# Performance work log

Hardware: AMD Instinct MI355X
Metric: run time of the kernel (lower is better)

## Reference

```python
import jax, jax.numpy as jnp
import numpy as np

HIDDEN = 2048
NUM_HEADS = 16
NUM_KV_HEADS = 4
HEAD_DIM = HIDDEN // NUM_HEADS  # 128
GROUP = NUM_HEADS // NUM_KV_HEADS  # 4
SCALE = HEAD_DIM ** -0.5


def setup_inputs() -> dict:
    key = jax.random.key(0)
    ks = jax.random.split(key, 9)
    B, S = 2, 2048
    kv_dim = HEAD_DIM * NUM_KV_HEADS
    std = HIDDEN ** -0.5
    return {
        "x": jax.random.normal(ks[0], (B, S, HIDDEN), dtype=jnp.float32),
        "Wq": jax.random.normal(ks[1], (HIDDEN, HIDDEN), dtype=jnp.float32) * std,
        "bq": jnp.zeros((HIDDEN,), dtype=jnp.float32),
        "Wk": jax.random.normal(ks[2], (HIDDEN, kv_dim), dtype=jnp.float32) * std,
        "bk": jnp.zeros((kv_dim,), dtype=jnp.float32),
        "Wv": jax.random.normal(ks[3], (HIDDEN, kv_dim), dtype=jnp.float32) * std,
        "bv": jnp.zeros((kv_dim,), dtype=jnp.float32),
        "Wo": jax.random.normal(ks[4], (HIDDEN, HIDDEN), dtype=jnp.float32) * std,
        "bo": jnp.zeros((HIDDEN,), dtype=jnp.float32),
    }


def reference(x, Wq, bq, Wk, bk, Wv, bv, Wo, bo):
    B, S, _ = x.shape
    # projections
    q = (x @ Wq + bq).reshape(B, S, NUM_KV_HEADS, GROUP, HEAD_DIM)  # grouped query heads
    k = (x @ Wk + bk).reshape(B, S, NUM_KV_HEADS, HEAD_DIM)
    v = (x @ Wv + bv).reshape(B, S, NUM_KV_HEADS, HEAD_DIM)
    # scores: [B, Hkv, G, Sq, Sk] -- same math as repeat_interleave of K/V over G,
    # but K/V are broadcast over the group axis instead of materialized.
    attn = jnp.einsum("bqhgd,bkhd->bhgqk", q, k) * SCALE
    attn = jax.nn.softmax(attn, axis=-1)
    out = jnp.einsum("bhgqk,bkhd->bqhgd", attn, v).reshape(B, S, HIDDEN)
    return out @ Wo + bo
```

## Files before the change

kernel.cpp:

```cpp
#include <hip/hip_runtime.h>


#define SEQ    2048
#define HIDDEN 2048

typedef __attribute__((ext_vector_type(8))) short v8s;
typedef __attribute__((ext_vector_type(4))) float v4f;

#define MFMA16(a,b,c) __builtin_amdgcn_mfma_f32_16x16x32_bf16((a),(b),(c),0,0,0)

__device__ __forceinline__ ushort f2b(float f){
  unsigned u = __float_as_uint(f);
  u += 0x7fffu + ((u >> 16) & 1u);
  return (ushort)(u >> 16);
}

__device__ __forceinline__ unsigned cvt_pk_bf16(float lo, float hi){
  unsigned r;
  asm("v_cvt_pk_bf16_f32 %0, %1, %2" : "=v"(r) : "v"(lo), "v"(hi));
  return r;
}

__device__ __forceinline__ void gload16(const void* g, void* l){
  __builtin_amdgcn_global_load_lds((const __attribute__((address_space(1))) void*)g,
                                   (__attribute__((address_space(3))) void*)l, 16, 0, 0);
}

#define WAIT_VM0   0x0F70
#define WAIT_VM2   0x0F72
#define WAIT_LGKM0 0xC07F

__global__ void k_conv(const float* __restrict__ in, ushort* __restrict__ out, int n){
  int i = (blockIdx.x*256 + threadIdx.x)*4;
  if (i >= n) return;
  float4 f = *(const float4*)(in + i);
  ushort4 u; u.x=f2b(f.x); u.y=f2b(f.y); u.z=f2b(f.z); u.w=f2b(f.w);
  *(ushort4*)(out + i) = u;
}

__global__ void k_tconv(const float* __restrict__ in, ushort* __restrict__ out,
                        int rows, int cols){
  __shared__ float t[32][33];
  int tx = threadIdx.x & 31, ty = threadIdx.x >> 5;
  int c0 = blockIdx.x*32, r0 = blockIdx.y*32;
#pragma unroll
  for (int i=0;i<4;i++) t[ty+i*8][tx] = in[(size_t)(r0+ty+i*8)*cols + c0+tx];
  __syncthreads();
#pragma unroll
  for (int i=0;i<4;i++) out[(size_t)(c0+ty+i*8)*rows + r0+tx] = f2b(t[tx][ty+i*8]);
}

__global__ void k_tv(const ushort* __restrict__ vb, ushort* __restrict__ vT){
  __shared__ ushort t[32][33];
  int tx = threadIdx.x & 31, ty = threadIdx.x >> 5;
  int s0 = blockIdx.x*32, d0 = blockIdx.y*32, bh = blockIdx.z;
  int b = bh >> 2, h = bh & 3;
  const ushort* src = vb + (size_t)b*SEQ*512 + h*128;
#pragma unroll
  for (int i=0;i<4;i++) t[ty+i*8][tx] = src[(size_t)(s0+ty+i*8)*512 + d0+tx];
  __syncthreads();
  ushort* dst = vT + (size_t)bh*128*SEQ;
#pragma unroll
  for (int i=0;i<4;i++) dst[(size_t)(d0+ty+i*8)*SEQ + s0+tx] = t[tx][ty+i*8];
}

#define GEMM256_MAIN(A_, Bt_)                                                          \
  __shared__ ushort sA[2][2][128*64], sB[2][2][128*64];                                \
  const int tid = threadIdx.x, lane = tid & 63, w = tid >> 6;                          \
  const int wm = w >> 2, wn = w & 3, lm = lane & 15, quad = lane >> 4;                 \
  const int wh = wn >> 1, wl = wn & 1, l3 = lane >> 3, l7m = lm & 7;                   \
  const int swz = ((lane & 7) ^ (l3 & 7)) * 8;                                         \
  const ushort* Ag = (A_); const ushort* Bg = (Bt_);                                   \
  v4f acc[8][4] = {};                                                                  \
  STG_A(0,0,0) STG_A(0,1,0) STG_B(0,0,0) STG_B(0,1,0) STG_A(1,0,1)                     \
  __builtin_amdgcn_s_waitcnt(WAIT_VM2);                                                \
  __builtin_amdgcn_s_barrier(); __builtin_amdgcn_sched_barrier(0);                     \
  for (int t = 0; t < 32; t++){                                                        \
    const int p = t & 1, pn = p ^ 1;                                                   \
    const int tn  = (t+1 < 32) ? t+1 : t;                                              \
    const int tnn = (t+2 < 32) ? t+2 : 31;                                             \
    v8s a0[4][2], a1[4][2], bb0[2][2], bb1[2][2];                                      \
                                                                              \
    _Pragma("unroll")                                                                  \
    for (int i=0;i<4;i++){ LDA(a0[i][0], i, 0) LDA(a0[i][1], i, 1) }                   \
    _Pragma("unroll")                                                                  \
    for (int j=0;j<2;j++){ LDB(bb0[j][0], j, 0) LDB(bb0[j][1], j, 1) }                 \
    STG_A(tn, 1, pn)                                                                   \
    __builtin_amdgcn_s_barrier(); __builtin_amdgcn_sched_barrier(0);                   \
    __builtin_amdgcn_s_waitcnt(WAIT_LGKM0); __builtin_amdgcn_sched_barrier(0);         \
    __builtin_amdgcn_s_setprio(1);                                                     \
    _Pragma("unroll")                                                                  \
    for (int ks=0;ks<2;ks++)                                                           \
      _Pragma("unroll")                                                                \
      for (int i=0;i<4;i++)                                                            \
        _Pragma("unroll")                                                              \
        for (int j=0;j<2;j++) acc[i][j] = MFMA16(a0[i][ks], bb0[j][ks], acc[i][j]);    \
    __builtin_amdgcn_s_setprio(0);                                                     \
    __builtin_amdgcn_s_barrier(); __builtin_amdgcn_sched_barrier(0);                   \
                                                                              \
    _Pragma("unroll")                                                                  \
    for (int j=0;j<2;j++){ LDB(bb1[j][0], j+2, 0) LDB(bb1[j][1], j+2, 1) }             \
    STG_B(tn, 0, pn)                                                                   \
    __builtin_amdgcn_s_barrier(); __builtin_amdgcn_sched_barrier(0);                   \
    __builtin_amdgcn_s_waitcnt(WAIT_LGKM0); __builtin_amdgcn_sched_barrier(0);         \
    __builtin_amdgcn_s_setprio(1);                                                     \
    _Pragma("unroll")                                                                  \
    for (int ks=0;ks<2;ks++)                                                           \
      _Pragma("unroll")                                                                \
      for (int i=0;i<4;i++)                                                            \
        _Pragma("unroll")                                                              \
        for (int j=0;j<2;j++) acc[i][j+2] = MFMA16(a0[i][ks], bb1[j][ks], acc[i][j+2]);\
    __builtin_amdgcn_s_setprio(0);                                                     \
    __builtin_amdgcn_s_barrier(); __builtin_amdgcn_sched_barrier(0);                   \
                                                                              \
    _Pragma("unroll")                                                                  \
    for (int i=0;i<4;i++){ LDA(a1[i][0], i+4, 0) LDA(a1[i][1], i+4, 1) }               \
    STG_B(tn, 1, pn)                                                                   \
    __builtin_amdgcn_s_barrier(); __builtin_amdgcn_sched_barrier(0);                   \
    __builtin_amdgcn_s_waitcnt(WAIT_LGKM0); __builtin_amdgcn_sched_barrier(0);         \
    __builtin_amdgcn_s_setprio(1);                                                     \
    _Pragma("unroll")                                                                  \
    for (int ks=0;ks<2;ks++)                                                           \
      _Pragma("unroll")                                                                \
      for (int i=0;i<4;i++)                                                            \
        _Pragma("unroll")                                                              \
        for (int j=0;j<2;j++) acc[i+4][j] = MFMA16(a1[i][ks], bb0[j][ks], acc[i+4][j]);\
    __builtin_amdgcn_s_setprio(0);                                                     \
    __builtin_amdgcn_s_barrier(); __builtin_amdgcn_sched_barrier(0);                   \
                  \
    STG_A(tnn, 0, p)                                                                   \
    __builtin_amdgcn_s_waitcnt(WAIT_VM2); __builtin_amdgcn_sched_barrier(0);           \
    __builtin_amdgcn_s_barrier(); __builtin_amdgcn_sched_barrier(0);                   \
    __builtin_amdgcn_s_setprio(1);                                                     \
    _Pragma("unroll")                                                                  \
    for (int ks=0;ks<2;ks++)                                                           \
      _Pragma("unroll")                                                                \
      for (int i=0;i<4;i++)                                                            \
        _Pragma("unroll")                                                              \
        for (int j=0;j<2;j++)                                                          \
          acc[i+4][j+2] = MFMA16(a1[i][ks], bb1[j][ks], acc[i+4][j+2]);                \
    __builtin_amdgcn_s_setprio(0);                                                     \
    __builtin_amdgcn_s_barrier(); __builtin_amdgcn_sched_barrier(0);                   \
  }

#define STG_A(t_, h_, buf_) { _Pragma("unroll") for (int i_=0;i_<2;i_++){              \
    int c_ = w*2 + i_;                                                                 \
    gload16(Ag + (size_t)(rowB + (h_)*128 + c_*8 + l3)*HIDDEN + (t_)*64 + swz,         \
            &sA[buf_][h_][c_*512 + lane*8]); } }
#define STG_B(t_, h_, buf_) { _Pragma("unroll") for (int i_=0;i_<2;i_++){              \
    int c_ = w*2 + i_;                                                                 \
    gload16(Bg + (size_t)(colB + (h_)*128 + c_*8 + l3)*HIDDEN + (t_)*64 + swz,         \
            &sB[buf_][h_][c_*512 + lane*8]); } }
#define LDA(dst_, i_, ks_) dst_ = *(const v8s*)(&sA[p][wm][((i_)*16+lm)*64 + ((((ks_)*4+quad))^l7m)*8]);
#define LDB(dst_, j_, ks_) dst_ = *(const v8s*)(&sB[p][wh][(wl*64 + (j_)*16+lm)*64 + ((((ks_)*4+quad))^l7m)*8]);

__global__ __launch_bounds__(512, 1) void k_gemm_qkv(
    const ushort* __restrict__ A, const ushort* __restrict__ Bt,
    const float* __restrict__ bq, const float* __restrict__ bk, const float* __restrict__ bv,
    ushort* __restrict__ qb, ushort* __restrict__ kb, ushort* __restrict__ vb){
  const int flat = blockIdx.x;
  const int nf = (flat & 7) * 24 + (flat >> 3);
  const int rowB = (nf & 15) * 256;
  const int colB = (nf >> 4) * 256;
  GEMM256_MAIN(A, Bt)
#pragma unroll
  for (int i=0;i<8;i++)
#pragma unroll
  for (int j=0;j<4;j++){
    int col = colB + wn*64 + j*16 + lm;
#pragma unroll
    for (int r=0;r<4;r++){
      int row = rowB + wm*128 + i*16 + quad*4 + r;
      float v = acc[i][j][r];
      if (col < 2048)      qb[(size_t)row*2048 + col]        = f2b(v + bq[col]);
      else if (col < 2560) kb[(size_t)row*512 + (col-2048)]  = f2b(v + bk[col-2048]);
      else                 vb[(size_t)row*512 + (col-2560)]  = f2b(v + bv[col-2560]);
    }
  }
}

__global__ __launch_bounds__(512, 1) void k_gemm_out(
    const ushort* __restrict__ A, const ushort* __restrict__ Bt,
    const float* __restrict__ bo, float* __restrict__ out){
  __shared__ ushort sA[2][128*64], sB[2][2][128*64];
  const int tid = threadIdx.x, lane = tid & 63, w = tid >> 6;
  const int wm = w >> 2, wn = w & 3, lm = lane & 15, quad = lane >> 4;
  const int wh = wn >> 1, wl = wn & 1, l3 = lane >> 3, l7m = lm & 7;
  const int swz = ((lane & 7) ^ (l3 & 7)) * 8;
  const int flat = blockIdx.x;
  const int nf = (flat & 7) * 32 + (flat >> 3);
  const int rowB = (nf & 31) * 128;
  const int colB = (nf >> 5) * 256;
  const ushort* Ag = A; const ushort* Bg = Bt;
  v4f acc[4][4] = {};

#define OSTG_A(t_, buf_) { _Pragma("unroll") for (int i_=0;i_<2;i_++){                 \
    int c_ = w*2 + i_;                                                                 \
    gload16(Ag + (size_t)(rowB + c_*8 + l3)*HIDDEN + (t_)*64 + swz,                    \
            &sA[buf_][c_*512 + lane*8]); } }
#define OSTG_B(t_, h_, buf_) { _Pragma("unroll") for (int i_=0;i_<2;i_++){             \
    int c_ = w*2 + i_;                                                                 \
    gload16(Bg + (size_t)(colB + (h_)*128 + c_*8 + l3)*HIDDEN + (t_)*64 + swz,         \
            &sB[buf_][h_][c_*512 + lane*8]); } }
#define OLDA(dst_, i_, ks_) dst_ = *(const v8s*)(&sA[p][(wm*64 + (i_)*16 + lm)*64 + ((((ks_)*4+quad))^l7m)*8]);
#define OLDB(dst_, j_, ks_) dst_ = *(const v8s*)(&sB[p][wh][(wl*64 + (j_)*16 + lm)*64 + ((((ks_)*4+quad))^l7m)*8]);

  OSTG_A(0,0) OSTG_B(0,0,0) OSTG_B(0,1,0) OSTG_A(1,1)
  __builtin_amdgcn_s_waitcnt(WAIT_VM2);
  __builtin_amdgcn_s_barrier(); __builtin_amdgcn_sched_barrier(0);
  for (int t = 0; t < 32; t++){
    const int p = t & 1, pn = p ^ 1;
    const int tn  = (t+1 < 32) ? t+1 : t;
    const int tnn = (t+2 < 32) ? t+2 : 31;
    v8s a[4][2], b0[2][2], b1[2][2];
#pragma unroll
    for (int i=0;i<4;i++){ OLDA(a[i][0], i, 0) OLDA(a[i][1], i, 1) }
#pragma unroll
    for (int j=0;j<2;j++){ OLDB(b0[j][0], j, 0) OLDB(b0[j][1], j, 1) }
    OSTG_B(tn, 0, pn)
    __builtin_amdgcn_s_barrier(); __builtin_amdgcn_sched_barrier(0);
    __builtin_amdgcn_s_waitcnt(WAIT_LGKM0); __builtin_amdgcn_sched_barrier(0);
    __builtin_amdgcn_s_setprio(1);
#pragma unroll
    for (int ks=0;ks<2;ks++)
#pragma unroll
      for (int i=0;i<4;i++)
#pragma unroll
        for (int j=0;j<2;j++) acc[i][j] = MFMA16(a[i][ks], b0[j][ks], acc[i][j]);
    __builtin_amdgcn_s_setprio(0);
    __builtin_amdgcn_s_barrier(); __builtin_amdgcn_sched_barrier(0);
#pragma unroll
    for (int j=0;j<2;j++){ OLDB(b1[j][0], j+2, 0) OLDB(b1[j][1], j+2, 1) }
    OSTG_B(tn, 1, pn) OSTG_A(tnn, p)
    __builtin_amdgcn_s_waitcnt(WAIT_VM2); __builtin_amdgcn_sched_barrier(0);
    __builtin_amdgcn_s_barrier(); __builtin_amdgcn_sched_barrier(0);
    __builtin_amdgcn_s_waitcnt(WAIT_LGKM0); __builtin_amdgcn_sched_barrier(0);
    __builtin_amdgcn_s_setprio(1);
#pragma unroll
    for (int ks=0;ks<2;ks++)
#pragma unroll
      for (int i=0;i<4;i++)
#pragma unroll
        for (int j=0;j<2;j++) acc[i][j+2] = MFMA16(a[i][ks], b1[j][ks], acc[i][j+2]);
    __builtin_amdgcn_s_setprio(0);
    __builtin_amdgcn_s_barrier(); __builtin_amdgcn_sched_barrier(0);
  }
#pragma unroll
  for (int i=0;i<4;i++)
#pragma unroll
  for (int j=0;j<4;j++){
    int col = colB + wn*64 + j*16 + lm;
#pragma unroll
    for (int r=0;r<4;r++){
      int row = rowB + wm*64 + i*16 + quad*4 + r;
      out[(size_t)row*2048 + col] = acc[i][j][r] + bo[col];
    }
  }
#undef OSTG_A
#undef OSTG_B
#undef OLDA
#undef OLDB
}

__global__ __launch_bounds__(512, 2) void k_attn(
    const ushort* __restrict__ qb, const ushort* __restrict__ kb,
    const ushort* __restrict__ vT, ushort* __restrict__ Ob){
  __shared__ ushort sK[2][64*128];
  __shared__ ushort sV[2][128*64];
  __shared__ ushort sP[8][1024];
  const int tid = threadIdx.x, lane = tid & 63, w = tid >> 6;
  const int lm = lane & 15, quad = lane >> 4, q8 = quad*8;
  const int pair = blockIdx.x & 7;
  const int hkv = pair & 3, b = pair >> 2;
  const int qt = (blockIdx.x >> 3) & 15, g = blockIdx.x >> 7;
  const int head = hkv*4 + g;
  const float C = 0.08838834764831845f * 1.4426950408889634f;

  const ushort* kbb = kb + (size_t)b*SEQ*512 + hkv*128;
  const ushort* vbb = vT + (size_t)(b*4+hkv)*128*SEQ;

  const int kk = lane >> 4, ksw = lane & 15;
  const int dd = lane >> 3, vsw = lane & 7;

#define STAGE_K(t, buf) { _Pragma("unroll") for (int i=0;i<2;i++){                     \
    int c = w*2 + i; int key = c*4 + kk; int wd = ksw ^ (key & 15);                    \
    gload16(kbb + (size_t)((t)*64 + key)*512 + wd*8, &sK[buf][c*512 + lane*8]); } }
#define STAGE_V(t, buf) { _Pragma("unroll") for (int i=0;i<2;i++){                     \
    int c = w*2 + i; int drow = c*8 + dd; int wd = vsw ^ dd;                           \
    gload16(vbb + (size_t)drow*SEQ + (t)*64 + wd*8, &sV[buf][c*512 + lane*8]); } }

  v8s qf[4];
#pragma unroll
  for (int ks=0; ks<4; ks++)
    qf[ks] = *(const v8s*)(qb + (size_t)(b*SEQ + qt*128 + w*16 + lm)*HIDDEN
                              + head*128 + ks*32 + q8);

  v4f o[8] = {};
  float lreg = 0.f;

  STAGE_K(0, 0)
  STAGE_V(0, 0)
  __builtin_amdgcn_s_waitcnt(WAIT_VM0);
  __syncthreads();

  for (int t=0; t<32; t++){
    const int cur = t & 1;
    if (t < 31) STAGE_K(t+1, cur^1)

    v4f sacc[4] = {};
#pragma unroll
    for (int ks=0; ks<4; ks++){
      v8s kf[4];
#pragma unroll
      for (int kt=0; kt<4; kt++)
        kf[kt] = *(const v8s*)(&sK[cur][(kt*16+lm)*128 + ((ks*4+quad)^lm)*8]);
      __builtin_amdgcn_s_setprio(1);
#pragma unroll
      for (int kt=0; kt<4; kt++)
        sacc[kt] = MFMA16(kf[kt], qf[ks], sacc[kt]);
      __builtin_amdgcn_s_setprio(0);
    }

    {
      float rs = 0.f;
#pragma unroll
      for (int kt=0; kt<4; kt++){
        float p0 = __builtin_amdgcn_exp2f(sacc[kt][0]*C);
        float p1 = __builtin_amdgcn_exp2f(sacc[kt][1]*C);
        float p2 = __builtin_amdgcn_exp2f(sacc[kt][2]*C);
        float p3 = __builtin_amdgcn_exp2f(sacc[kt][3]*C);
        rs += (p0+p1)+(p2+p3);
        uint2 pk;
        pk.x = cvt_pk_bf16(p0, p1);
        pk.y = cvt_pk_bf16(p2, p3);
        int kc = kt >> 1;
        int dl = ((kt&1)*2 + (quad>>1))*16 + lm;
        *(uint2*)(&sP[w][kc*512 + dl*8 + (quad&1)*4]) = pk;
      }
      lreg += rs;
    }

    __builtin_amdgcn_s_waitcnt(WAIT_VM0);
    __syncthreads();
    if (t < 31) STAGE_V(t+1, cur^1)

    __builtin_amdgcn_s_waitcnt(WAIT_LGKM0);
    v8s pa[2];
#pragma unroll
    for (int kc=0; kc<2; kc++)
      pa[kc] = *(const v8s*)(&sP[w][kc*512 + lane*8]);
#pragma unroll
    for (int kc=0; kc<2; kc++){
      v8s vf[8];
#pragma unroll
      for (int dt=0; dt<8; dt++)
        vf[dt] = *(const v8s*)(&sV[cur][(dt*16+lm)*64 + ((kc*4+quad)^(lm&7))*8]);
      __builtin_amdgcn_s_setprio(1);
#pragma unroll
      for (int dt=0; dt<8; dt++)
        o[dt] = MFMA16(pa[kc], vf[dt], o[dt]);
      __builtin_amdgcn_s_setprio(0);
    }
  }

  {
    float lv = lreg;
    lv += __shfl_xor(lv, 16);
    lv += __shfl_xor(lv, 32);
    float inv[4];
#pragma unroll
    for (int r=0;r<4;r++) inv[r] = 1.0f / __shfl(lv, (lane & 48) + quad*4 + r);
#pragma unroll
    for (int dt=0; dt<8; dt++)
#pragma unroll
      for (int r=0;r<4;r++){
        int row = b*SEQ + qt*128 + w*16 + quad*4 + r;
        int col = head*128 + dt*16 + lm;
        Ob[(size_t)row*HIDDEN + col] = f2b(o[dt][r]*inv[r]);
      }
  }
#undef STAGE_K
#undef STAGE_V
}

extern "C" void kernel_launch(void* const* d_in, const int* in_sizes, int n_in,
                              void* d_out, int out_size, void* d_ws, size_t ws_size,
                              hipStream_t stream){
  const float* x  = (const float*)d_in[0];
  const float* Wq = (const float*)d_in[1];
  const float* bq = (const float*)d_in[2];
  const float* Wk = (const float*)d_in[3];
  const float* bk = (const float*)d_in[4];
  const float* Wv = (const float*)d_in[5];
  const float* bv = (const float*)d_in[6];
  const float* Wo = (const float*)d_in[7];
  const float* bo = (const float*)d_in[8];
  float* out = (float*)d_out;

  ushort* xb  = (ushort*)d_ws;
  ushort* Wt  = xb  + 8388608;
  ushort* Wto = Wt  + 6291456;
  ushort* qb  = Wto + 4194304;
  ushort* kb  = qb  + 8388608;
  ushort* vb  = kb  + 2097152;
  ushort* vT  = vb  + 2097152;
  ushort* Ob  = vT  + 2097152;

  k_conv <<<8192, 256, 0, stream>>>(x, xb, 8388608);
  k_tconv<<<dim3(64,64), 256, 0, stream>>>(Wq, Wt, 2048, 2048);
  k_tconv<<<dim3(16,64), 256, 0, stream>>>(Wk, Wt + 4194304, 2048, 512);
  k_tconv<<<dim3(16,64), 256, 0, stream>>>(Wv, Wt + 5242880, 2048, 512);
  k_tconv<<<dim3(64,64), 256, 0, stream>>>(Wo, Wto, 2048, 2048);
  k_gemm_qkv<<<192, 512, 0, stream>>>(xb, Wt, bq, bk, bv, qb, kb, vb);
  k_tv  <<<dim3(64,4,8), 256, 0, stream>>>(vb, vT);
  k_attn<<<512, 512, 0, stream>>>(qb, kb, vT, Ob);
  k_gemm_out<<<256, 512, 0, stream>>>(Ob, Wto, bo, out);
}
```

Baseline: 346.7 us.

## Merge conversion kernels into one launch and simplify GEMM block mapping

Replaces the x conversion kernel and the four weight transpose-conversion launches with a single k_prep kernel that picks its job from the block index, removing four kernel launches and their gaps. Separately, the QKV and output GEMMs drop their XCD-aware swizzled block index mapping in favour of a plain 2D grid. That simpler mapping may change how tiles are spread across chiplets and hurt L2 reuse.

```diff
diff --git a/kernel.cpp b/kernel.cpp
--- a/kernel.cpp
+++ b/kernel.cpp
@@ -30,19 +30,28 @@
 #define WAIT_VM2   0x0F72
 #define WAIT_LGKM0 0xC07F
 
-__global__ void k_conv(const float* __restrict__ in, ushort* __restrict__ out, int n){
-  int i = (blockIdx.x*256 + threadIdx.x)*4;
-  if (i >= n) return;
-  float4 f = *(const float4*)(in + i);
-  ushort4 u; u.x=f2b(f.x); u.y=f2b(f.y); u.z=f2b(f.z); u.w=f2b(f.w);
-  *(ushort4*)(out + i) = u;
-}
-
-__global__ void k_tconv(const float* __restrict__ in, ushort* __restrict__ out,
-                        int rows, int cols){
+__global__ __launch_bounds__(256) void k_prep(
+    const float* __restrict__ x,  const float* __restrict__ Wq,
+    const float* __restrict__ Wk, const float* __restrict__ Wv,
+    const float* __restrict__ Wo, ushort* __restrict__ xb,
+    ushort* __restrict__ Wt, ushort* __restrict__ Wto){
   __shared__ float t[32][33];
+  int id = blockIdx.x;
+  if (id < 8192){
+    int i = (id*256 + threadIdx.x)*4;
+    float4 f = *(const float4*)(x + i);
+    ushort4 u; u.x=f2b(f.x); u.y=f2b(f.y); u.z=f2b(f.z); u.w=f2b(f.w);
+    *(ushort4*)(xb + i) = u;
+    return;
+  }
+  id -= 8192;
+  const float* in; ushort* out; int rows, cols, bx, by;
+  if (id < 4096)      { in=Wq; out=Wt;           rows=2048; cols=2048; bx=id&63; by=id>>6; }
+  else if (id < 5120) { id-=4096; in=Wk; out=Wt+4194304; rows=2048; cols=512; bx=id&15; by=id>>4; }
+  else if (id < 6144) { id-=5120; in=Wv; out=Wt+5242880; rows=2048; cols=512; bx=id&15; by=id>>4; }
+  else                { id-=6144; in=Wo; out=Wto;         rows=2048; cols=2048; bx=id&63; by=id>>6; }
   int tx = threadIdx.x & 31, ty = threadIdx.x >> 5;
-  int c0 = blockIdx.x*32, r0 = blockIdx.y*32;
+  int c0 = bx*32, r0 = by*32;
 #pragma unroll
   for (int i=0;i<4;i++) t[ty+i*8][tx] = in[(size_t)(r0+ty+i*8)*cols + c0+tx];
   __syncthreads();
@@ -158,10 +167,7 @@
     const ushort* __restrict__ A, const ushort* __restrict__ Bt,
     const float* __restrict__ bq, const float* __restrict__ bk, const float* __restrict__ bv,
     ushort* __restrict__ qb, ushort* __restrict__ kb, ushort* __restrict__ vb){
-  const int flat = blockIdx.x;
-  const int nf = (flat & 7) * 24 + (flat >> 3);
-  const int rowB = (nf & 15) * 256;
-  const int colB = (nf >> 4) * 256;
+  const int rowB = blockIdx.y*256, colB = blockIdx.x*256;
   GEMM256_MAIN(A, Bt)
 #pragma unroll
   for (int i=0;i<8;i++)
@@ -187,10 +193,7 @@
   const int wm = w >> 2, wn = w & 3, lm = lane & 15, quad = lane >> 4;
   const int wh = wn >> 1, wl = wn & 1, l3 = lane >> 3, l7m = lm & 7;
   const int swz = ((lane & 7) ^ (l3 & 7)) * 8;
-  const int flat = blockIdx.x;
-  const int nf = (flat & 7) * 32 + (flat >> 3);
-  const int rowB = (nf & 31) * 128;
-  const int colB = (nf >> 5) * 256;
+  const int rowB = blockIdx.y*128, colB = blockIdx.x*256;
   const ushort* Ag = A; const ushort* Bg = Bt;
   v4f acc[4][4] = {};
 
@@ -406,13 +409,9 @@
   ushort* vT  = vb  + 2097152;
   ushort* Ob  = vT  + 2097152;
 
-  k_conv <<<8192, 256, 0, stream>>>(x, xb, 8388608);
-  k_tconv<<<dim3(64,64), 256, 0, stream>>>(Wq, Wt, 2048, 2048);
-  k_tconv<<<dim3(16,64), 256, 0, stream>>>(Wk, Wt + 4194304, 2048, 512);
-  k_tconv<<<dim3(16,64), 256, 0, stream>>>(Wv, Wt + 5242880, 2048, 512);
-  k_tconv<<<dim3(64,64), 256, 0, stream>>>(Wo, Wto, 2048, 2048);
-  k_gemm_qkv<<<192, 512, 0, stream>>>(xb, Wt, bq, bk, bv, qb, kb, vb);
+  k_prep<<<18432, 256, 0, stream>>>(x, Wq, Wk, Wv, Wo, xb, Wt, Wto);
+  k_gemm_qkv<<<dim3(12,16), 512, 0, stream>>>(xb, Wt, bq, bk, bv, qb, kb, vb);
   k_tv  <<<dim3(64,4,8), 256, 0, stream>>>(vb, vT);
   k_attn<<<512, 512, 0, stream>>>(qb, kb, vT, Ob);
-  k_gemm_out<<<256, 512, 0, stream>>>(Ob, Wto, bo, out);
-}
+  k_gemm_out<<<dim3(8,32), 512, 0, stream>>>(Ob, Wto, bo, out);
+}
```

Result: faster. 339.0 us (-2.2%).
